# Performance work log

Measured on AMD Instinct MI355X. Metric: run time of the kernel, lower is better.

The kernel has to match this reference:

```python
import jax, jax.numpy as jnp
import numpy as np

INPUT_DIM = 128
HIDDEN_DIM = 512
STACK_DIM = 64
BATCH = 128
MAX_T = 259  # 2*128 + 3
SEQ_L = 259  # l, so k = (l-3)//2 = 128


def setup_inputs() -> dict:
    key = jax.random.key(0)
    ks = jax.random.split(key, 7)
    G = 4 * HIDDEN_DIM
    x = jax.random.normal(ks[0], (SEQ_L, BATCH, INPUT_DIM), dtype=jnp.float32)
    Wih = jax.random.normal(ks[1], (G, INPUT_DIM + STACK_DIM), dtype=jnp.float32) * 0.05
    bih = jax.random.normal(ks[2], (G,), dtype=jnp.float32) * 0.05
    Whh = jax.random.normal(ks[3], (G, HIDDEN_DIM), dtype=jnp.float32) * 0.05
    bhh = jax.random.normal(ks[4], (G,), dtype=jnp.float32) * 0.05
    Wr = jax.random.normal(ks[5], (INPUT_DIM + STACK_DIM + 2, HIDDEN_DIM), dtype=jnp.float32) * 0.05
    br = jax.random.normal(ks[6], (INPUT_DIM + STACK_DIM + 2,), dtype=jnp.float32) * 0.05
    return {"x": x, "Wih": Wih, "bih": bih, "Whh": Whh, "bhh": bhh, "Wr": Wr, "br": br}


def _forward(x, Wih, bih, Whh, bhh, Wr, br):
    l = x.shape[0]
    k = (l - 3) // 2
    B = x.shape[1]

    def lstm_cell(xin, h, c):
        # torch.nn.LSTMCell: gate order i, f, g, o
        g = xin @ Wih.T + bih + h @ Whh.T + bhh  # [B, 4H]
        i, f, gg, o = jnp.split(g, 4, axis=1)
        c2 = jax.nn.sigmoid(f) * c + jax.nn.sigmoid(i) * jnp.tanh(gg)
        h2 = jax.nn.sigmoid(o) * jnp.tanh(c2)
        return h2, c2

    def update_stack(V, s, vt, ut, dt, t):
        Vp = V.at[:, t, :].add(vt)  # scatter vt into row t (row was zero)
        # baddbmm with strict-upper-triangular ones matrix == suffix sum:
        # prod[b, i] = sum_{j > i} s[b, j]
        prod = jnp.cumsum(s[:, ::-1], axis=1)[:, ::-1] - s
        sp = jnp.maximum(0.0, s - jnp.maximum(0.0, ut - prod))
        sp = sp.at[:, t].set(dt[:, 0])
        inner = jax.nn.relu(1.0 - prod - sp)  # uses prod from OLD s, as in source
        A = jnp.minimum(sp, inner)  # [B, MAX_T]
        rt = jnp.einsum('bt,btd->bd', A, Vp)
        return Vp, sp, rt

    def step(carry, inp):
        V, s, h, c, rt = carry
        xt, t = inp
        h, c = lstm_cell(jnp.concatenate([xt, rt], axis=1), h, c)
        out = h @ Wr.T + br  # [B, S + I + 2]
        vt = out[:, :STACK_DIM]
        ot = out[:, STACK_DIM:STACK_DIM + INPUT_DIM]
        ut = jax.nn.sigmoid(out[:, STACK_DIM + INPUT_DIM:STACK_DIM + INPUT_DIM + 1])
        dt = jax.nn.sigmoid(out[:, STACK_DIM + INPUT_DIM + 1:])
        V, s, rt = update_stack(V, s, vt, ut, dt, t)
        return (V, s, h, c, rt), ot

    dt_ = x.dtype
    carry = (jnp.zeros((B, MAX_T, STACK_DIM), dt_),
             jnp.zeros((B, MAX_T), dt_),
             jnp.zeros((B, HIDDEN_DIM), dt_),
             jnp.zeros((B, HIDDEN_DIM), dt_),
             jnp.zeros((B, STACK_DIM), dt_))
    # encode phase: steps 0..k with real inputs (outputs discarded)
    carry, _ = jax.lax.scan(step, carry, (x[:k + 1], jnp.arange(k + 1)))
    # decode phase: steps k+1..2k+2 with zero inputs (same encode_LSTM, per source)
    xz = jnp.zeros((k + 2, B, INPUT_DIM), dt_)
    carry, ots = jax.lax.scan(step, carry, (xz, k + 1 + jnp.arange(k + 2)))
    return jax.nn.log_softmax(ots, axis=2)  # [k+2, B, INPUT_DIM]


def reference(x, Wih, bih, Whh, bhh, Wr, br):
    return _forward(x, Wih, bih, Whh, bhh, Wr, br)
```

## Files before the change

kernel.cpp:

```cpp
#include <hip/hip_runtime.h>
#include <hip/hip_bf16.h>
#include <math.h>

#define IDIM 128
#define HDIM 512
#define SDIM 64
#define BATCH 128
#define MAXT 259
#define G4 2048
#define KTOT 704
#define ROUT 194
#define AFRAG_U 73728
#define NBLK 256
#define NGATE 16
#define PTJ 224
#define PCJ 80
#define POJ 128

typedef __hip_bfloat16 bf16;
typedef __attribute__((ext_vector_type(8))) short short8;
typedef __attribute__((ext_vector_type(4))) float floatx4;

__device__ __forceinline__ float sigmoidf_(float v) { return 1.f / (1.f + expf(-v)); }
__device__ __forceinline__ float b2f(bf16 v) { return __bfloat162float(v); }
__device__ __forceinline__ float load_in(const void* p, size_t i, int isf32) {
    return isf32 ? ((const float*)p)[i] : b2f(((const bf16*)p)[i]);
}
__device__ __forceinline__ unsigned short f2bfbits(float v) {
    unsigned u = __builtin_bit_cast(unsigned, v);
    unsigned r = (u + 0x7FFFu + ((u >> 16) & 1u)) >> 16;
    return (unsigned short)r;
}
__device__ __forceinline__ float bfbits2f(unsigned short b) {
    return __builtin_bit_cast(float, (unsigned)b << 16);
}
__device__ __forceinline__ unsigned aload(const unsigned* p) {
    return __hip_atomic_load(p, __ATOMIC_RELAXED, __HIP_MEMORY_SCOPE_AGENT);
}
__device__ __forceinline__ unsigned long long aload64(const unsigned long long* p) {
    return __hip_atomic_load(p, __ATOMIC_RELAXED, __HIP_MEMORY_SCOPE_AGENT);
}
__device__ __forceinline__ void astore32(unsigned* p, unsigned v) {
    __hip_atomic_store(p, v, __ATOMIC_RELAXED, __HIP_MEMORY_SCOPE_AGENT);
}
__device__ __forceinline__ void astore64(unsigned long long* p, unsigned long long v) {
    __hip_atomic_store(p, v, __ATOMIC_RELAXED, __HIP_MEMORY_SCOPE_AGENT);
}
__device__ __forceinline__ unsigned long long packf2(float a, float b) {
    return (unsigned long long)__builtin_bit_cast(unsigned, a)
         | ((unsigned long long)__builtin_bit_cast(unsigned, b) << 32);
}
__device__ __forceinline__ void unpack_frag(const unsigned long long* ap,
                                            short8& ah, short8& al) {
    #pragma unroll
    for (int j = 0; j < 4; j++) {
        unsigned long long q = aload64(ap + j);
        unsigned u0 = (unsigned)q, u1 = (unsigned)(q >> 32);
        ah[2 * j]     = (short)(u0 & 0xffffu);
        al[2 * j]     = (short)(u0 >> 16);
        ah[2 * j + 1] = (short)(u1 & 0xffffu);
        al[2 * j + 1] = (short)(u1 >> 16);
    }
}

__device__ __forceinline__ void wait_flags16(const unsigned* f, int base16,
                                             unsigned tgt) {
    if (threadIdx.x < 16) {
        while (aload(&f[(base16 + (int)threadIdx.x) * 16]) < tgt)
            __builtin_amdgcn_s_sleep(1);
    }
    __atomic_signal_fence(__ATOMIC_SEQ_CST);
    __syncthreads();
}

__global__ void detect_kernel(const unsigned short* __restrict__ w, int* __restrict__ flag) {
    if (threadIdx.x == 0) {
        int isf32 = 0;
        for (int i = 0; i < 256; i++) {
            int e = (w[i] >> 7) & 0xFF;
            if (e >= 0x8F) isf32 = 1;
        }
        *flag = isf32;
    }
}

__global__ void prep_kernel(const void* __restrict__ Wih, const void* __restrict__ bih,
                            const void* __restrict__ Whh, const void* __restrict__ bhh,
                            unsigned short* __restrict__ WfH, unsigned short* __restrict__ WfL,
                            float* __restrict__ bc, const int* __restrict__ flag) {
    int isf32 = *flag;
    int jp = blockIdx.x;
    int u = jp >> 2, gate = jp & 3;
    int src = gate * HDIM + u;
    int jt = jp >> 4, jn = jp & 15;
    for (int k = threadIdx.x; k < KTOT; k += blockDim.x) {
        float v = (k < 192) ? load_in(Wih, (size_t)src * 192 + k, isf32)
                            : load_in(Whh, (size_t)src * HDIM + (k - 192), isf32);
        unsigned short hi = f2bfbits(v);
        unsigned short lo = f2bfbits(v - bfbits2f(hi));
        int ks = k >> 5, q = (k & 31) >> 3, e = k & 7;
        size_t d = (((size_t)jt * 22 + ks) * 64 + (q * 16 + jn)) * 8 + e;
        WfH[d] = hi;
        WfL[d] = lo;
    }
    if (threadIdx.x == 0)
        bc[jp] = load_in(bih, src, isf32) + load_in(bhh, src, isf32);
}

__global__ void wr_prep_kernel(const void* __restrict__ Wr, const void* __restrict__ br,
                               unsigned short* __restrict__ WrBh, unsigned short* __restrict__ WrBl,
                               float* __restrict__ brf, const int* __restrict__ flag) {
    int isf32 = *flag;
    int j = blockIdx.x;
    for (int k = threadIdx.x; k < HDIM; k += blockDim.x) {
        float v = (j < ROUT) ? load_in(Wr, (size_t)j * HDIM + k, isf32) : 0.f;
        unsigned short hi = f2bfbits(v);
        WrBh[(size_t)j * HDIM + k] = hi;
        WrBl[(size_t)j * HDIM + k] = f2bfbits(v - bfbits2f(hi));
    }
    if (threadIdx.x == 0) brf[j] = (j < ROUT) ? load_in(br, j, isf32) : 0.f;
}

__global__ __launch_bounds__(256) void persist_kernel(
        const void* __restrict__ x,
        const unsigned short* __restrict__ WfH, const unsigned short* __restrict__ WfL,
        const float* __restrict__ bc,
        const unsigned short* __restrict__ WrBh, const unsigned short* __restrict__ WrBl,
        const float* __restrict__ brf,
        unsigned* __restrict__ AfP,
        float* __restrict__ partC,
        float* __restrict__ partO,
        unsigned short* __restrict__ Vg,
        void* __restrict__ dout, const int* __restrict__ flag,
        unsigned* __restrict__ hfl, unsigned* __restrict__ pfl,
        unsigned* __restrict__ rtf, unsigned* __restrict__ oflg) {
    __shared__ __align__(16) short Ahs[18 * 64 * 8];
    __shared__ __align__(16) short Als[18 * 64 * 8];
    __shared__ __align__(16) unsigned short wrslB[14 * 64 * 8];
    __shared__ __align__(16) unsigned short wrslBL[14 * 64 * 8];
    __shared__ __align__(16) float scr[8][16][20];
    __shared__ __align__(16) unsigned short hlh[16 * 40];
    __shared__ __align__(16) unsigned short hll[16 * 40];
    __shared__ __align__(16) float outsC[80];
    __shared__ __align__(16) float sL[324];
    __shared__ __align__(16) float aL[324];
    __shared__ __align__(16) float red[4][64];
    __shared__ __align__(16) float redo[128][2];
    __shared__ __align__(16) float oL[128];
    __shared__ __align__(16) float brS[208];
    __shared__ __align__(16) float bcS[128];
    __shared__ int e0S;

    const int tid = threadIdx.x, lane = tid & 63, wv = tid >> 6;
    const int blk = blockIdx.x, ms = blk >> 5, ns = blk & 31;
    const int isf32 = *flag;
    float* const pt = (float*)Ahs;

    const int is_gate = (ns < 16);
    const int gb = ns;
    const int pb = ns - 16;
    const int p2row = ms * 16 + pb;

    if (is_gate) {
        for (int i = tid; i < 14 * 64 * 8; i += 256) {
            int jt = i >> 9, l = (i >> 3) & 63, e = i & 7;
            size_t src = (size_t)(jt * 16 + (l & 15)) * HDIM + gb * 32 + (l >> 4) * 8 + e;
            wrslB[i]  = WrBh[src];
            wrslBL[i] = WrBl[src];
        }
        if (tid < 128) bcS[tid] = bc[gb * 128 + tid];
    } else {
        for (int i = tid; i < 208; i += 256) brS[i] = brf[i];
        for (int i = tid; i < 324; i += 256) { sL[i] = 0.f; aL[i] = 0.f; }
    }
    __syncthreads();

    if (is_gate) {
        const short8* WH = (const short8*)WfH;
        const short8* WL = (const short8*)WfL;
        const int jt0 = gb * 8 + wv, jt1 = gb * 8 + 4 + wv;
        const short8* wb0  = WH + (size_t)jt0 * 22 * 64;
        const short8* wb1  = WH + (size_t)jt1 * 22 * 64;
        const short8* wbl0 = WL + (size_t)jt0 * 22 * 64;
        const short8* wbl1 = WL + (size_t)jt1 * 22 * 64;
        float cc0 = 0.f, cc1 = 0.f;

        for (int t = 0; t < MAXT; t++) {
            const int cur = t & 1, nxt = cur ^ 1;
            const unsigned long long* AfPc64 =
                (const unsigned long long*)(AfP + (size_t)cur * AFRAG_U);
            unsigned long long* AfPn64 =
                (unsigned long long*)(AfP + (size_t)nxt * AFRAG_U);
            const int use_x = (t < 129);

            floatx4 acc0 = {0.f, 0.f, 0.f, 0.f};
            floatx4 acc1 = {0.f, 0.f, 0.f, 0.f};
            if (use_x) {
                int m = lane & 15, q = lane >> 4;
                size_t xrow = ((size_t)t * BATCH + ms * 16 + m) * IDIM + q * 8;
                #pragma unroll
                for (int ks = 0; ks < 4; ks++) {
                    short8 a;
                    if (isf32) {
                        const float* xf = (const float*)x + xrow + ks * 32;
                        #pragma unroll
                        for (int i = 0; i < 8; i++) a[i] = (short)f2bfbits(xf[i]);
                    } else {
                        a = *(const short8*)((const unsigned short*)x + xrow + ks * 32);
                    }
                    acc0 = __builtin_amdgcn_mfma_f32_16x16x32_bf16(a, wb0[ks * 64 + lane], acc0, 0, 0, 0);
                    acc1 = __builtin_amdgcn_mfma_f32_16x16x32_bf16(a, wb1[ks * 64 + lane], acc1, 0, 0, 0);
                    if (isf32) {
                        acc0 = __builtin_amdgcn_mfma_f32_16x16x32_bf16(a, wbl0[ks * 64 + lane], acc0, 0, 0, 0);
                        acc1 = __builtin_amdgcn_mfma_f32_16x16x32_bf16(a, wbl1[ks * 64 + lane], acc1, 0, 0, 0);
                    }
                }
            }

            wait_flags16(hfl, ms * 16, (unsigned)t);
            #pragma unroll
            for (int i0 = 0; i0 < 4; i0++) {
                int i = i0 * 256 + tid;
                int ksi = 2 + (i >> 6), l = i & 63;
                const unsigned long long* ap =
                    AfPc64 + ((size_t)(ms * 18 + ksi) * 64 + l) * 4;
                short8 ah, al8;
                unpack_frag(ap, ah, al8);
                *(short8*)&Ahs[(ksi * 64 + l) * 8] = ah;
                *(short8*)&Als[(ksi * 64 + l) * 8] = al8;
            }
            __syncthreads();

            #pragma unroll 4
            for (int ksi = 2; ksi < 18; ksi++) {
                int ks = 4 + ksi;
                short8 ah  = *(const short8*)&Ahs[(ksi * 64 + lane) * 8];
                short8 al8 = *(const short8*)&Als[(ksi * 64 + lane) * 8];
                short8 bh0 = wb0[ks * 64 + lane];
                short8 bh1 = wb1[ks * 64 + lane];
                acc0 = __builtin_amdgcn_mfma_f32_16x16x32_bf16(ah, bh0, acc0, 0, 0, 0);
                acc0 = __builtin_amdgcn_mfma_f32_16x16x32_bf16(al8, bh0, acc0, 0, 0, 0);
                acc1 = __builtin_amdgcn_mfma_f32_16x16x32_bf16(ah, bh1, acc1, 0, 0, 0);
                acc1 = __builtin_amdgcn_mfma_f32_16x16x32_bf16(al8, bh1, acc1, 0, 0, 0);
                if (isf32) {
                    acc0 = __builtin_amdgcn_mfma_f32_16x16x32_bf16(ah, wbl0[ks * 64 + lane], acc0, 0, 0, 0);
                    acc1 = __builtin_amdgcn_mfma_f32_16x16x32_bf16(ah, wbl1[ks * 64 + lane], acc1, 0, 0, 0);
                }
            }

            wait_flags16(rtf, ms * 16, (unsigned)t);
            if (tid < 128) {
                int ksi = tid >> 6, l = tid & 63;
                const unsigned long long* ap =
                    AfPc64 + ((size_t)(ms * 18 + ksi) * 64 + l) * 4;
                short8 ah, al8;
                unpack_frag(ap, ah, al8);
                *(short8*)&Ahs[(ksi * 64 + l) * 8] = ah;
                *(short8*)&Als[(ksi * 64 + l) * 8] = al8;
            }
            __syncthreads();
            #pragma unroll
            for (int ksi = 0; ksi < 2; ksi++) {
                int ks = 4 + ksi;
                short8 ah  = *(const short8*)&Ahs[(ksi * 64 + lane) * 8];
                short8 al8 = *(const short8*)&Als[(ksi * 64 + lane) * 8];
                short8 bh0 = wb0[ks * 64 + lane];
                short8 bh1 = wb1[ks * 64 + lane];
                acc0 = __builtin_amdgcn_mfma_f32_16x16x32_bf16(ah, bh0, acc0, 0, 0, 0);
                acc0 = __builtin_amdgcn_mfma_f32_16x16x32_bf16(al8, bh0, acc0, 0, 0, 0);
                acc1 = __builtin_amdgcn_mfma_f32_16x16x32_bf16(ah, bh1, acc1, 0, 0, 0);
                acc1 = __builtin_amdgcn_mfma_f32_16x16x32_bf16(al8, bh1, acc1, 0, 0, 0);
                if (isf32) {
                    acc0 = __builtin_amdgcn_mfma_f32_16x16x32_bf16(ah, wbl0[ks * 64 + lane], acc0, 0, 0, 0);
                    acc1 = __builtin_amdgcn_mfma_f32_16x16x32_bf16(ah, wbl1[ks * 64 + lane], acc1, 0, 0, 0);
                }
            }
            {
                int n = lane & 15, m0 = (lane >> 4) * 4;
                #pragma unroll
                for (int r = 0; r < 4; r++) scr[wv][m0 + r][n] = acc0[r];
                #pragma unroll
                for (int r = 0; r < 4; r++) scr[wv + 4][m0 + r][n] = acc1[r];
            }
            __syncthreads();
            {
                int r = tid >> 4, p = tid & 15;
                float4 g = *(const float4*)&scr[p >> 2][r][(p & 3) * 4];
                float4 bb = *(const float4*)&bcS[p * 4];
                float c2 = sigmoidf_(g.y + bb.y) * cc0 + sigmoidf_(g.x + bb.x) * tanhf(g.z + bb.z);
                float h2 = sigmoidf_(g.w + bb.w) * tanhf(c2);
                cc0 = c2;
                unsigned short hi0 = f2bfbits(h2);
                hlh[r * 40 + p] = hi0;
                hll[r * 40 + p] = f2bfbits(h2 - bfbits2f(hi0));
                int u1 = p + 16;
                float4 g1 = *(const float4*)&scr[u1 >> 2][r][(u1 & 3) * 4];
                float4 bb1 = *(const float4*)&bcS[u1 * 4];
                float c21 = sigmoidf_(g1.y + bb1.y) * cc1 + sigmoidf_(g1.x + bb1.x) * tanhf(g1.z + bb1.z);
                float h21 = sigmoidf_(g1.w + bb1.w) * tanhf(c21);
                cc1 = c21;
                unsigned short hi1 = f2bfbits(h21);
                hlh[r * 40 + u1] = hi1;
                hll[r * 40 + u1] = f2bfbits(h21 - bfbits2f(hi1));
            }
            __syncthreads();

            {
                int m = lane & 15, q = lane >> 4;
                short8 ahh = *(const short8*)&hlh[m * 40 + q * 8];
                short8 ahl = *(const short8*)&hll[m * 40 + q * 8];
                int n = lane & 15, m0 = (lane >> 4) * 4;
                {
                    const short8* bB  = (const short8*)&wrslB[((size_t)wv * 64 + lane) * 8];
                    const short8* bBl = (const short8*)&wrslBL[((size_t)wv * 64 + lane) * 8];
                    floatx4 accR = {0.f, 0.f, 0.f, 0.f};
                    short8 bh = *bB;
                    accR = __builtin_amdgcn_mfma_f32_16x16x32_bf16(ahh, bh, accR, 0, 0, 0);
                    accR = __builtin_amdgcn_mfma_f32_16x16x32_bf16(ahl, bh, accR, 0, 0, 0);
                    if (isf32) {
                        short8 bl = *bBl;
                        accR = __builtin_amdgcn_mfma_f32_16x16x32_bf16(ahh, bl, accR, 0, 0, 0);
                        accR = __builtin_amdgcn_mfma_f32_16x16x32_bf16(ahl, bl, accR, 0, 0, 0);
                    }
                    #pragma unroll
                    for (int r = 0; r < 4; r++) {
                        int row = ms * 16 + m0 + r;
                        astore32((unsigned*)partC + ((size_t)row * NGATE + gb) * PCJ
                                     + wv * 16 + n,
                                 __builtin_bit_cast(unsigned, accR[r]));
                    }
                }
                if (wv == 0) {
                    const short8* bB  = (const short8*)&wrslB[((size_t)12 * 64 + lane) * 8];
                    const short8* bBl = (const short8*)&wrslBL[((size_t)12 * 64 + lane) * 8];
                    floatx4 accR = {0.f, 0.f, 0.f, 0.f};
                    short8 bh = *bB;
                    accR = __builtin_amdgcn_mfma_f32_16x16x32_bf16(ahh, bh, accR, 0, 0, 0);
                    accR = __builtin_amdgcn_mfma_f32_16x16x32_bf16(ahl, bh, accR, 0, 0, 0);
                    if (isf32) {
                        short8 bl = *bBl;
                        accR = __builtin_amdgcn_mfma_f32_16x16x32_bf16(ahh, bl, accR, 0, 0, 0);
                        accR = __builtin_amdgcn_mfma_f32_16x16x32_bf16(ahl, bl, accR, 0, 0, 0);
                    }
                    if (n < 2) {
                        #pragma unroll
                        for (int r = 0; r < 4; r++) {
                            int row = ms * 16 + m0 + r;
                            astore32((unsigned*)partC + ((size_t)row * NGATE + gb) * PCJ
                                         + 64 + n,
                                     __builtin_bit_cast(unsigned, accR[r]));
                        }
                    }
                }
            }
            asm volatile("s_waitcnt vmcnt(0)" ::: "memory");
            __syncthreads();
            if (tid == 0)
                __hip_atomic_store(&pfl[(ms * 16 + gb) * 16], (unsigned)(t + 1),
                                   __ATOMIC_RELAXED, __HIP_MEMORY_SCOPE_AGENT);

            {
                int rr = tid >> 4, pp = tid & 15;
                unsigned short hb0 = hlh[rr * 40 + 2 * pp];
                unsigned short lb0 = hll[rr * 40 + 2 * pp];
                unsigned short hb1 = hlh[rr * 40 + 2 * pp + 1];
                unsigned short lb1 = hll[rr * 40 + 2 * pp + 1];
                unsigned u0 = (unsigned)hb0 | ((unsigned)lb0 << 16);
                unsigned u1 = (unsigned)hb1 | ((unsigned)lb1 << 16);
                int u_g = gb * 32 + 2 * pp;
                int ksi2 = 2 + (u_g >> 5), q = (u_g & 31) >> 3, e = u_g & 7;
                size_t fi = (((size_t)ms * 18 + ksi2) * 64 + q * 16 + rr) * 8 + e;
                astore64(AfPn64 + fi / 2, (unsigned long long)u0 | ((unsigned long long)u1 << 32));
            }
            asm volatile("s_waitcnt vmcnt(0)" ::: "memory");
            __syncthreads();
            if (tid == 0)
                __hip_atomic_store(&hfl[(ms * 16 + gb) * 16], (unsigned)(t + 1),
                                   __ATOMIC_RELAXED, __HIP_MEMORY_SCOPE_AGENT);

            if (!use_x) {
                {
                    int m = lane & 15, q = lane >> 4;
                    short8 ahh = *(const short8*)&hlh[m * 40 + q * 8];
                    short8 ahl = *(const short8*)&hll[m * 40 + q * 8];
                    int n = lane & 15, m0 = (lane >> 4) * 4;
                    #pragma unroll
                    for (int s2 = 0; s2 < 2; s2++) {
                        int jt = 4 + wv + s2 * 4;
                        const short8* bB  = (const short8*)&wrslB[((size_t)jt * 64 + lane) * 8];
                        const short8* bBl = (const short8*)&wrslBL[((size_t)jt * 64 + lane) * 8];
                        floatx4 accR = {0.f, 0.f, 0.f, 0.f};
                        short8 bh = *bB;
                        accR = __builtin_amdgcn_mfma_f32_16x16x32_bf16(ahh, bh, accR, 0, 0, 0);
                        accR = __builtin_amdgcn_mfma_f32_16x16x32_bf16(ahl, bh, accR, 0, 0, 0);
                        if (isf32) {
                            short8 bl = *bBl;
                            accR = __builtin_amdgcn_mfma_f32_16x16x32_bf16(ahh, bl, accR, 0, 0, 0);
                            accR = __builtin_amdgcn_mfma_f32_16x16x32_bf16(ahl, bl, accR, 0, 0, 0);
                        }
                        #pragma unroll
                        for (int ri = 0; ri < 4; ri++)
                            pt[(m0 + ri) * PTJ + jt * 16 + n] = accR[ri];
                    }
                }
                __syncthreads();
                {
                    #pragma unroll
                    for (int it = 0; it < 4; it++) {
                        int rloc = wv * 4 + it;
                        int prow_ = ms * 16 + rloc;
                        const float* pr = pt + rloc * PTJ;
                        unsigned long long* pb64 = (unsigned long long*)
                            (partO + ((((size_t)cur * BATCH + prow_) * NGATE) + gb) * POJ);
                        astore64(pb64 + lane, packf2(pr[64 + 2 * lane], pr[65 + 2 * lane]));
                    }
                }
                asm volatile("s_waitcnt vmcnt(0)" ::: "memory");
                __syncthreads();
                if (tid == 0)
                    __hip_atomic_store(&oflg[(ms * 16 + gb) * 16], (unsigned)(t + 1),
                                       __ATOMIC_RELAXED, __HIP_MEMORY_SCOPE_AGENT);
            }
        }
    } else {
        unsigned short* Vrow = Vg + (size_t)p2row * MAXT * SDIM;
        for (int t = 0; t < MAXT; t++) {
            unsigned long long* AfPn64 =
                (unsigned long long*)(AfP + (size_t)((t + 1) & 1) * AFRAG_U);

            wait_flags16(pfl, ms * 16, (unsigned)(t + 1));

            if (tid < 66) {
                const unsigned* pb2 = (const unsigned*)partC
                                    + (size_t)p2row * NGATE * PCJ + tid;
                float s4 = (tid < 64) ? brS[tid] : brS[128 + tid];
                #pragma unroll
                for (int g = 0; g < NGATE; g++)
                    s4 += __builtin_bit_cast(float, aload(pb2 + (size_t)g * PCJ));
                outsC[tid] = s4;
            }
            __syncthreads();
            if (wv == 0) {
                float uval = sigmoidf_(outsC[64]);
                float dval = sigmoidf_(outsC[65]);
                Vrow[t * SDIM + lane] = f2bfbits(outsC[lane]);
                int ebase = lane * 5;
                float sv[5], suf[5];
                #pragma unroll
                for (int j = 0; j < 5; j++) {
                    int e = ebase + j;
                    sv[j] = (e < MAXT) ? sL[e] : 0.f;
                }
                suf[4] = sv[4];
                #pragma unroll
                for (int j = 3; j >= 0; j--) suf[j] = sv[j] + suf[j + 1];
                float ltot = suf[0];
                float accs = ltot;
                #pragma unroll
                for (int off = 1; off < 64; off <<= 1) {
                    float y = __shfl_down(accs, off, 64);
                    if (lane + off < 64) accs += y;
                }
                float after_lane = accs - ltot;
                int emin = 0x7fffffff;
                #pragma unroll
                for (int j = 0; j < 5; j++) {
                    int e = ebase + j;
                    if (e <= t) {
                        float prod = after_lane + (suf[j] - sv[j]);
                        float sp = (e == t) ? dval
                                            : fmaxf(0.f, sv[j] - fmaxf(0.f, uval - prod));
                        float inner = fmaxf(0.f, 1.f - prod - sp);
                        sL[e] = sp;
                        aL[e] = fminf(sp, inner);
                        if (prod < 1.f && e < emin) emin = e;
                    }
                }
                #pragma unroll
                for (int off = 32; off; off >>= 1) {
                    int o = __shfl_xor(emin, off, 64);
                    emin = o < emin ? o : emin;
                }
                if (lane == 0) e0S = emin;
            }
            __syncthreads();
            const int e0 = e0S;
            float rtv = 0.f;
            if (e0 > t - 16) {
                if (wv == 0) {
                    for (int i2 = e0; i2 <= t; i2++)
                        rtv += aL[i2] * bfbits2f(Vrow[i2 * SDIM + lane]);
                }
            } else {
                float racc = 0.f;
                int i2s = e0 + ((wv - e0) & 3);
                for (int i2 = i2s; i2 <= t; i2 += 4)
                    racc += aL[i2] * bfbits2f(Vrow[i2 * SDIM + lane]);
                red[wv][lane] = racc;
                __syncthreads();
                if (wv == 0)
                    rtv = red[0][lane] + red[1][lane] + red[2][lane] + red[3][lane];
            }
            if (wv == 0) {
                float rtn = __shfl_down(rtv, 1, 64);
                if ((lane & 1) == 0) {
                    unsigned short hb0 = f2bfbits(rtv);
                    unsigned short lb0 = f2bfbits(rtv - bfbits2f(hb0));
                    unsigned short hb1 = f2bfbits(rtn);
                    unsigned short lb1 = f2bfbits(rtn - bfbits2f(hb1));
                    unsigned u0 = (unsigned)hb0 | ((unsigned)lb0 << 16);
                    unsigned u1 = (unsigned)hb1 | ((unsigned)lb1 << 16);
                    int d0 = lane;
                    int ksi = d0 >> 5, q = (d0 & 31) >> 3, e = d0 & 7;
                    size_t fi = (((size_t)ms * 18 + ksi) * 64 + q * 16 + pb) * 8 + e;
                    astore64(AfPn64 + fi / 2,
                             (unsigned long long)u0 | ((unsigned long long)u1 << 32));
                }
                asm volatile("s_waitcnt vmcnt(0)" ::: "memory");
                if (lane == 0)
                    __hip_atomic_store(&rtf[(ms * 16 + pb) * 16], (unsigned)(t + 1),
                                       __ATOMIC_RELAXED, __HIP_MEMORY_SCOPE_AGENT);
            }
            if (t >= 129) {
                wait_flags16(oflg, ms * 16, (unsigned)(t + 1));
                {
                    int col = tid >> 1, half = tid & 1;
                    const unsigned* pbo = (const unsigned*)partO
                        + (((size_t)(t & 1) * BATCH + p2row) * NGATE) * POJ + col;
                    float s = 0.f;
                    #pragma unroll
                    for (int g = 0; g < 8; g++)
                        s += __builtin_bit_cast(float,
                                aload(pbo + (size_t)(half * 8 + g) * POJ));
                    redo[col][half] = s;
                }
                __syncthreads();
                if (tid < 128) oL[tid] = redo[tid][0] + redo[tid][1] + brS[64 + tid];
                __syncthreads();
                if (wv == 0) {
                    float a = oL[lane];
                    float bvv = oL[64 + lane];
                    float m = fmaxf(a, bvv);
                    #pragma unroll
                    for (int off = 32; off; off >>= 1) m = fmaxf(m, __shfl_xor(m, off, 64));
                    float e = expf(a - m) + expf(bvv - m);
                    #pragma unroll
                    for (int off = 32; off; off >>= 1) e += __shfl_xor(e, off, 64);
                    float ls = logf(e) + m;
                    size_t base = ((size_t)(t - 129) * BATCH + p2row) * IDIM;
                    if (isf32) {
                        ((float*)dout)[base + lane] = a - ls;
                        ((float*)dout)[base + lane + 64] = bvv - ls;
                    } else {
                        ((bf16*)dout)[base + lane] = __float2bfloat16(a - ls);
                        ((bf16*)dout)[base + lane + 64] = __float2bfloat16(bvv - ls);
                    }
                }
            }
        }
    }
}

extern "C" void kernel_launch(void* const* d_in, const int* in_sizes, int n_in,
                              void* d_out, int out_size, void* d_ws, size_t ws_size,
                              hipStream_t stream) {
    const void* x   = d_in[0];
    const void* Wih = d_in[1];
    const void* bih = d_in[2];
    const void* Whh = d_in[3];
    const void* bhh = d_in[4];
    const void* Wr  = d_in[5];
    const void* br  = d_in[6];

    char* base = (char*)d_ws;
    size_t off = 0;
    int* flag = (int*)base;                                   off += 64;
    unsigned* hfl = (unsigned*)(base + off);                  off += 128 * 64 + 64;
    unsigned* pfl = (unsigned*)(base + off);                  off += 128 * 64 + 64;
    unsigned* rtf = (unsigned*)(base + off);                  off += 128 * 64 + 64;
    unsigned* oflg = (unsigned*)(base + off);                 off += 128 * 64 + 64;
    unsigned short* WfH  = (unsigned short*)(base + off);     off += (size_t)G4 * KTOT * 2;
    unsigned short* WfL  = (unsigned short*)(base + off);     off += (size_t)G4 * KTOT * 2;
    unsigned short* WrBh = (unsigned short*)(base + off);     off += (size_t)224 * HDIM * 2;
    unsigned short* WrBl = (unsigned short*)(base + off);     off += (size_t)224 * HDIM * 2;
    float* bc   = (float*)(base + off);                       off += G4 * 4;
    float* brf  = (float*)(base + off);                       off += 1024;
    unsigned* AfP = (unsigned*)(base + off);                  size_t af_off = off;
                                                              off += (size_t)2 * AFRAG_U * 4;
    float* partC = (float*)(base + off);                      off += (size_t)BATCH * NGATE * PCJ * 4;
    float* partO = (float*)(base + off);                      off += (size_t)2 * BATCH * NGATE * POJ * 4;
    unsigned short* Vg = (unsigned short*)(base + off);       off += (size_t)BATCH * MAXT * SDIM * 2;

    hipMemsetAsync(base + 64, 0, 4 * (128 * 64 + 64), stream);
    hipMemsetAsync(base + af_off, 0, (size_t)2 * AFRAG_U * 4, stream);
    hipMemsetAsync(partC, 0, (size_t)BATCH * NGATE * PCJ * 4, stream);

    detect_kernel<<<1, 64, 0, stream>>>((const unsigned short*)Wih, flag);
    prep_kernel<<<G4, 256, 0, stream>>>(Wih, bih, Whh, bhh, WfH, WfL, bc, flag);
    wr_prep_kernel<<<224, 256, 0, stream>>>(Wr, br, WrBh, WrBl, brf, flag);

    persist_kernel<<<NBLK, 256, 0, stream>>>(x, WfH, WfL, bc, WrBh, WrBl, brf,
                                             AfP, partC, partO, Vg, d_out, flag,
                                             hfl, pfl, rtf, oflg);

    (void)in_sizes; (void)n_in; (void)out_size; (void)ws_size;
}
```

Baseline: 2.983 ms.

## Publish hidden state fragments right after LSTM cell, drop extra barrier phase

Each thread now writes its packed hi/lo bf16 hidden values straight into the global A-fragment buffer as soon as the LSTM cell computes them. The h-ready flag is raised before the output projection instead of after it, and a separate repack-from-LDS pass with its own wait and barrier is removed. This lets consumer blocks start the next recurrent step sooner. The stack read is also made uniform, always splitting across four waves with a shared reduction, which trades a branch for a barrier on short stacks.

Result: no change. 2.990 ms (+0.2%).

```diff
diff --git a/kernel.cpp b/kernel.cpp
--- a/kernel.cpp
+++ b/kernel.cpp
@@ -291,8 +291,9 @@
                 float h2 = sigmoidf_(g.w + bb.w) * tanhf(c2);
                 cc0 = c2;
                 unsigned short hi0 = f2bfbits(h2);
+                unsigned short lo0 = f2bfbits(h2 - bfbits2f(hi0));
                 hlh[r * 40 + p] = hi0;
-                hll[r * 40 + p] = f2bfbits(h2 - bfbits2f(hi0));
+                hll[r * 40 + p] = lo0;
                 int u1 = p + 16;
                 float4 g1 = *(const float4*)&scr[u1 >> 2][r][(u1 & 3) * 4];
                 float4 bb1 = *(const float4*)&bcS[u1 * 4];
@@ -300,10 +301,21 @@
                 float h21 = sigmoidf_(g1.w + bb1.w) * tanhf(c21);
                 cc1 = c21;
                 unsigned short hi1 = f2bfbits(h21);
+                unsigned short lo1 = f2bfbits(h21 - bfbits2f(hi1));
                 hlh[r * 40 + u1] = hi1;
-                hll[r * 40 + u1] = f2bfbits(h21 - bfbits2f(hi1));
-            }
-            __syncthreads();
+                hll[r * 40 + u1] = lo1;
+                unsigned* AfPn32 = (unsigned*)AfPn64;
+                size_t fb = ((size_t)ms * 18 + 2 + gb) * 64;
+                size_t fi1 = (fb + (size_t)((p >> 3) * 16 + r)) * 8 + (p & 7);
+                size_t fi2 = (fb + (size_t)((2 + (p >> 3)) * 16 + r)) * 8 + (p & 7);
+                astore32(AfPn32 + fi1, (unsigned)hi0 | ((unsigned)lo0 << 16));
+                astore32(AfPn32 + fi2, (unsigned)hi1 | ((unsigned)lo1 << 16));
+            }
+            asm volatile("s_waitcnt vmcnt(0)" ::: "memory");
+            __syncthreads();
+            if (tid == 0)
+                __hip_atomic_store(&hfl[(ms * 16 + gb) * 16], (unsigned)(t + 1),
+                                   __ATOMIC_RELAXED, __HIP_MEMORY_SCOPE_AGENT);
 
             {
                 int m = lane & 15, q = lane >> 4;
@@ -357,25 +369,6 @@
             __syncthreads();
             if (tid == 0)
                 __hip_atomic_store(&pfl[(ms * 16 + gb) * 16], (unsigned)(t + 1),
-                                   __ATOMIC_RELAXED, __HIP_MEMORY_SCOPE_AGENT);
-
-            {
-                int rr = tid >> 4, pp = tid & 15;
-                unsigned short hb0 = hlh[rr * 40 + 2 * pp];
-                unsigned short lb0 = hll[rr * 40 + 2 * pp];
-                unsigned short hb1 = hlh[rr * 40 + 2 * pp + 1];
-                unsigned short lb1 = hll[rr * 40 + 2 * pp + 1];
-                unsigned u0 = (unsigned)hb0 | ((unsigned)lb0 << 16);
-                unsigned u1 = (unsigned)hb1 | ((unsigned)lb1 << 16);
-                int u_g = gb * 32 + 2 * pp;
-                int ksi2 = 2 + (u_g >> 5), q = (u_g & 31) >> 3, e = u_g & 7;
-                size_t fi = (((size_t)ms * 18 + ksi2) * 64 + q * 16 + rr) * 8 + e;
-                astore64(AfPn64 + fi / 2, (unsigned long long)u0 | ((unsigned long long)u1 << 32));
-            }
-            asm volatile("s_waitcnt vmcnt(0)" ::: "memory");
-            __syncthreads();
-            if (tid == 0)
-                __hip_atomic_store(&hfl[(ms * 16 + gb) * 16], (unsigned)(t + 1),
                                    __ATOMIC_RELAXED, __HIP_MEMORY_SCOPE_AGENT);
 
             if (!use_x) {
@@ -484,24 +477,19 @@
                 if (lane == 0) e0S = emin;
             }
             __syncthreads();
-            const int e0 = e0S;
-            float rtv = 0.f;
-            if (e0 > t - 16) {
-                if (wv == 0) {
-                    for (int i2 = e0; i2 <= t; i2++)
-                        rtv += aL[i2] * bfbits2f(Vrow[i2 * SDIM + lane]);
-                }
-            } else {
+            {
+                const int e0 = e0S;
                 float racc = 0.f;
-                int i2s = e0 + ((wv - e0) & 3);
-                for (int i2 = i2s; i2 <= t; i2 += 4)
-                    racc += aL[i2] * bfbits2f(Vrow[i2 * SDIM + lane]);
+                if (e0 <= t) {
+                    int i2s = e0 + ((wv - e0) & 3);
+                    for (int i2 = i2s; i2 <= t; i2 += 4)
+                        racc += aL[i2] * bfbits2f(Vrow[i2 * SDIM + lane]);
+                }
                 red[wv][lane] = racc;
-                __syncthreads();
-                if (wv == 0)
-                    rtv = red[0][lane] + red[1][lane] + red[2][lane] + red[3][lane];
-            }
+            }
+            __syncthreads();
             if (wv == 0) {
+                float rtv = red[0][lane] + red[1][lane] + red[2][lane] + red[3][lane];
                 float rtn = __shfl_down(rtv, 1, 64);
                 if ((lane & 1) == 0) {
                     unsigned short hb0 = f2bfbits(rtv);
```

## Move output projection from gate blocks into stack blocks, dropping partO and oflg

Applied to the files above, without the earlier changes.

Gate blocks no longer compute the decode-phase output logits with MFMA and publish partial sums through partO plus a separate flag. Instead, each stack block waits on the h flags, rebuilds the full 512-wide h row from the split-bf16 fragment buffer, and computes the 128 output logits itself with scalar dot products over Wr read from global memory. This takes work and a synchronisation round off the gate blocks' critical path, and the read-vector reduction is made uniform across the four waves. In exchange, the stack blocks do more scalar work and global weight reads for every decode step.

After: 3.207 ms. 7.5% more time.

```diff
diff --git a/kernel.cpp b/kernel.cpp
--- a/kernel.cpp
+++ b/kernel.cpp
@@ -13,9 +13,7 @@
 #define AFRAG_U 73728
 #define NBLK 256
 #define NGATE 16
-#define PTJ 224
 #define PCJ 80
-#define POJ 128
 
 typedef __hip_bfloat16 bf16;
 typedef __attribute__((ext_vector_type(8))) short short8;
@@ -45,10 +43,6 @@
 }
 __device__ __forceinline__ void astore64(unsigned long long* p, unsigned long long v) {
     __hip_atomic_store(p, v, __ATOMIC_RELAXED, __HIP_MEMORY_SCOPE_AGENT);
-}
-__device__ __forceinline__ unsigned long long packf2(float a, float b) {
-    return (unsigned long long)__builtin_bit_cast(unsigned, a)
-         | ((unsigned long long)__builtin_bit_cast(unsigned, b) << 32);
 }
 __device__ __forceinline__ void unpack_frag(const unsigned long long* ap,
                                             short8& ah, short8& al) {
@@ -129,11 +123,10 @@
         const float* __restrict__ brf,
         unsigned* __restrict__ AfP,
         float* __restrict__ partC,
-        float* __restrict__ partO,
         unsigned short* __restrict__ Vg,
         void* __restrict__ dout, const int* __restrict__ flag,
         unsigned* __restrict__ hfl, unsigned* __restrict__ pfl,
-        unsigned* __restrict__ rtf, unsigned* __restrict__ oflg) {
+        unsigned* __restrict__ rtf) {
     __shared__ __align__(16) short Ahs[18 * 64 * 8];
     __shared__ __align__(16) short Als[18 * 64 * 8];
     __shared__ __align__(16) unsigned short wrslB[14 * 64 * 8];
@@ -141,11 +134,12 @@
     __shared__ __align__(16) float scr[8][16][20];
     __shared__ __align__(16) unsigned short hlh[16 * 40];
     __shared__ __align__(16) unsigned short hll[16 * 40];
+    __shared__ __align__(16) float hL[512];
     __shared__ __align__(16) float outsC[80];
     __shared__ __align__(16) float sL[324];
     __shared__ __align__(16) float aL[324];
     __shared__ __align__(16) float red[4][64];
-    __shared__ __align__(16) float redo[128][2];
+    __shared__ __align__(16) float oLp[128][2];
     __shared__ __align__(16) float oL[128];
     __shared__ __align__(16) float brS[208];
     __shared__ __align__(16) float bcS[128];
@@ -154,7 +148,6 @@
     const int tid = threadIdx.x, lane = tid & 63, wv = tid >> 6;
     const int blk = blockIdx.x, ms = blk >> 5, ns = blk & 31;
     const int isf32 = *flag;
-    float* const pt = (float*)Ahs;
 
     const int is_gate = (ns < 16);
     const int gb = ns;
@@ -377,50 +370,6 @@
             if (tid == 0)
                 __hip_atomic_store(&hfl[(ms * 16 + gb) * 16], (unsigned)(t + 1),
                                    __ATOMIC_RELAXED, __HIP_MEMORY_SCOPE_AGENT);
-
-            if (!use_x) {
-                {
-                    int m = lane & 15, q = lane >> 4;
-                    short8 ahh = *(const short8*)&hlh[m * 40 + q * 8];
-                    short8 ahl = *(const short8*)&hll[m * 40 + q * 8];
-                    int n = lane & 15, m0 = (lane >> 4) * 4;
-                    #pragma unroll
-                    for (int s2 = 0; s2 < 2; s2++) {
-                        int jt = 4 + wv + s2 * 4;
-                        const short8* bB  = (const short8*)&wrslB[((size_t)jt * 64 + lane) * 8];
-                        const short8* bBl = (const short8*)&wrslBL[((size_t)jt * 64 + lane) * 8];
-                        floatx4 accR = {0.f, 0.f, 0.f, 0.f};
-                        short8 bh = *bB;
-                        accR = __builtin_amdgcn_mfma_f32_16x16x32_bf16(ahh, bh, accR, 0, 0, 0);
-                        accR = __builtin_amdgcn_mfma_f32_16x16x32_bf16(ahl, bh, accR, 0, 0, 0);
-                        if (isf32) {
-                            short8 bl = *bBl;
-                            accR = __builtin_amdgcn_mfma_f32_16x16x32_bf16(ahh, bl, accR, 0, 0, 0);
-                            accR = __builtin_amdgcn_mfma_f32_16x16x32_bf16(ahl, bl, accR, 0, 0, 0);
-                        }
-                        #pragma unroll
-                        for (int ri = 0; ri < 4; ri++)
-                            pt[(m0 + ri) * PTJ + jt * 16 + n] = accR[ri];
-                    }
-                }
-                __syncthreads();
-                {
-                    #pragma unroll
-                    for (int it = 0; it < 4; it++) {
-                        int rloc = wv * 4 + it;
-                        int prow_ = ms * 16 + rloc;
-                        const float* pr = pt + rloc * PTJ;
-                        unsigned long long* pb64 = (unsigned long long*)
-                            (partO + ((((size_t)cur * BATCH + prow_) * NGATE) + gb) * POJ);
-                        astore64(pb64 + lane, packf2(pr[64 + 2 * lane], pr[65 + 2 * lane]));
-                    }
-                }
-                asm volatile("s_waitcnt vmcnt(0)" ::: "memory");
-                __syncthreads();
-                if (tid == 0)
-                    __hip_atomic_store(&oflg[(ms * 16 + gb) * 16], (unsigned)(t + 1),
-                                       __ATOMIC_RELAXED, __HIP_MEMORY_SCOPE_AGENT);
-            }
         }
     } else {
         unsigned short* Vrow = Vg + (size_t)p2row * MAXT * SDIM;
@@ -484,24 +433,19 @@
                 if (lane == 0) e0S = emin;
             }
             __syncthreads();
-            const int e0 = e0S;
-            float rtv = 0.f;
-            if (e0 > t - 16) {
-                if (wv == 0) {
-                    for (int i2 = e0; i2 <= t; i2++)
-                        rtv += aL[i2] * bfbits2f(Vrow[i2 * SDIM + lane]);
-                }
-            } else {
+            {
+                const int e0 = e0S;
                 float racc = 0.f;
-                int i2s = e0 + ((wv - e0) & 3);
-                for (int i2 = i2s; i2 <= t; i2 += 4)
-                    racc += aL[i2] * bfbits2f(Vrow[i2 * SDIM + lane]);
+                if (e0 <= t) {
+                    int i2s = e0 + ((wv - e0) & 3);
+                    for (int i2 = i2s; i2 <= t; i2 += 4)
+                        racc += aL[i2] * bfbits2f(Vrow[i2 * SDIM + lane]);
+                }
                 red[wv][lane] = racc;
-                __syncthreads();
-                if (wv == 0)
-                    rtv = red[0][lane] + red[1][lane] + red[2][lane] + red[3][lane];
-            }
+            }
+            __syncthreads();
             if (wv == 0) {
+                float rtv = red[0][lane] + red[1][lane] + red[2][lane] + red[3][lane];
                 float rtn = __shfl_down(rtv, 1, 64);
                 if ((lane & 1) == 0) {
                     unsigned short hb0 = f2bfbits(rtv);
@@ -521,21 +465,55 @@
                     __hip_atomic_store(&rtf[(ms * 16 + pb) * 16], (unsigned)(t + 1),
                                        __ATOMIC_RELAXED, __HIP_MEMORY_SCOPE_AGENT);
             }
+
             if (t >= 129) {
-                wait_flags16(oflg, ms * 16, (unsigned)(t + 1));
+                wait_flags16(hfl, ms * 16, (unsigned)(t + 1));
                 {
-                    int col = tid >> 1, half = tid & 1;
-                    const unsigned* pbo = (const unsigned*)partO
-                        + (((size_t)(t & 1) * BATCH + p2row) * NGATE) * POJ + col;
+                    const unsigned* Afn32 =
+                        (const unsigned*)(AfP + (size_t)((t + 1) & 1) * AFRAG_U);
+                    int u = 2 * tid;
+                    size_t fi = (((size_t)ms * 18 + 2 + (u >> 5)) * 64
+                                 + (size_t)(((u & 31) >> 3) * 16 + pb)) * 8 + (u & 7);
+                    unsigned long long q =
+                        aload64((const unsigned long long*)Afn32 + fi / 2);
+                    unsigned w0 = (unsigned)q, w1 = (unsigned)(q >> 32);
+                    hL[u]     = bfbits2f((unsigned short)(w0 & 0xffffu))
+                              + bfbits2f((unsigned short)(w0 >> 16));
+                    hL[u + 1] = bfbits2f((unsigned short)(w1 & 0xffffu))
+                              + bfbits2f((unsigned short)(w1 >> 16));
+                }
+                __syncthreads();
+                {
+                    int j = tid >> 1, ks0 = (tid & 1) * 256;
+                    const unsigned short* wr = WrBh + (size_t)(64 + j) * HDIM + ks0;
                     float s = 0.f;
-                    #pragma unroll
-                    for (int g = 0; g < 8; g++)
-                        s += __builtin_bit_cast(float,
-                                aload(pbo + (size_t)(half * 8 + g) * POJ));
-                    redo[col][half] = s;
+                    #pragma unroll 4
+                    for (int k0 = 0; k0 < 256; k0 += 8) {
+                        short8 w = *(const short8*)(wr + k0);
+                        float4 hv0 = *(const float4*)&hL[ks0 + k0];
+                        float4 hv1 = *(const float4*)&hL[ks0 + k0 + 4];
+                        s += bfbits2f((unsigned short)w[0]) * hv0.x + bfbits2f((unsigned short)w[1]) * hv0.y
+                           + bfbits2f((unsigned short)w[2]) * hv0.z + bfbits2f((unsigned short)w[3]) * hv0.w
+                           + bfbits2f((unsigned short)w[4]) * hv1.x + bfbits2f((unsigned short)w[5]) * hv1.y
+                           + bfbits2f((unsigned short)w[6]) * hv1.z + bfbits2f((unsigned short)w[7]) * hv1.w;
+                    }
+                    if (isf32) {
+                        const unsigned short* wrl = WrBl + (size_t)(64 + j) * HDIM + ks0;
+                        #pragma unroll 4
+                        for (int k0 = 0; k0 < 256; k0 += 8) {
+                            short8 w = *(const short8*)(wrl + k0);
+                            float4 hv0 = *(const float4*)&hL[ks0 + k0];
+                            float4 hv1 = *(const float4*)&hL[ks0 + k0 + 4];
+                            s += bfbits2f((unsigned short)w[0]) * hv0.x + bfbits2f((unsigned short)w[1]) * hv0.y
+                               + bfbits2f((unsigned short)w[2]) * hv0.z + bfbits2f((unsigned short)w[3]) * hv0.w
+                               + bfbits2f((unsigned short)w[4]) * hv1.x + bfbits2f((unsigned short)w[5]) * hv1.y
+                               + bfbits2f((unsigned short)w[6]) * hv1.z + bfbits2f((unsigned short)w[7]) * hv1.w;
+                        }
+                    }
+                    oLp[j][tid & 1] = s;
                 }
                 __syncthreads();
-                if (tid < 128) oL[tid] = redo[tid][0] + redo[tid][1] + brS[64 + tid];
+                if (tid < 128) oL[tid] = oLp[tid][0] + oLp[tid][1] + brS[64 + tid];
                 __syncthreads();
                 if (wv == 0) {
                     float a = oL[lane];
@@ -578,7 +556,6 @@
     unsigned* hfl = (unsigned*)(base + off);                  off += 128 * 64 + 64;
     unsigned* pfl = (unsigned*)(base + off);                  off += 128 * 64 + 64;
     unsigned* rtf = (unsigned*)(base + off);                  off += 128 * 64 + 64;
-    unsigned* oflg = (unsigned*)(base + off);                 off += 128 * 64 + 64;
     unsigned short* WfH  = (unsigned short*)(base + off);     off += (size_t)G4 * KTOT * 2;
     unsigned short* WfL  = (unsigned short*)(base + off);     off += (size_t)G4 * KTOT * 2;
     unsigned short* WrBh = (unsigned short*)(base + off);     off += (size_t)224 * HDIM * 2;
@@ -588,10 +565,9 @@
     unsigned* AfP = (unsigned*)(base + off);                  size_t af_off = off;
                                                               off += (size_t)2 * AFRAG_U * 4;
     float* partC = (float*)(base + off);                      off += (size_t)BATCH * NGATE * PCJ * 4;
-    float* partO = (float*)(base + off);                      off += (size_t)2 * BATCH * NGATE * POJ * 4;
     unsigned short* Vg = (unsigned short*)(base + off);       off += (size_t)BATCH * MAXT * SDIM * 2;
 
-    hipMemsetAsync(base + 64, 0, 4 * (128 * 64 + 64), stream);
+    hipMemsetAsync(base + 64, 0, 3 * (128 * 64 + 64), stream);
     hipMemsetAsync(base + af_off, 0, (size_t)2 * AFRAG_U * 4, stream);
     hipMemsetAsync(partC, 0, (size_t)BATCH * NGATE * PCJ * 4, stream);
 
@@ -600,8 +576,8 @@
     wr_prep_kernel<<<224, 256, 0, stream>>>(Wr, br, WrBh, WrBl, brf, flag);
 
     persist_kernel<<<NBLK, 256, 0, stream>>>(x, WfH, WfL, bc, WrBh, WrBl, brf,
-                                             AfP, partC, partO, Vg, d_out, flag,
-                                             hfl, pfl, rtf, oflg);
+                                             AfP, partC, Vg, d_out, flag,
+                                             hfl, pfl, rtf);
 
     (void)in_sizes; (void)n_in; (void)out_size; (void)ws_size;
 }
```
